# Kernel optimization log

Measured on AMD Instinct MI355X. Metric: run time of the kernel, lower is better.

Reference implementation:

```python
import jax, jax.numpy as jnp
import numpy as np

D_MODEL = 48
SSM_RATIO = 2
D_INNER = D_MODEL * SSM_RATIO   # 96
D_STATE = 16
DT_RANK = -(-D_MODEL // 16)     # ceil(48/16) = 3
K = 4                           # 4 scan directions
LAP_ITERS = 10
LAP_TAU = 0.1
B, DD, HH, WW = 2, 20, 20, 20   # L = 8000 (even)


def _lap_kernel(c):
    k = np.zeros((3, 3, 3), dtype=np.float32)
    k[1, 1, 1] = -6.0
    k[0, 1, 1] = k[2, 1, 1] = 1.0
    k[1, 0, 1] = k[1, 2, 1] = 1.0
    k[1, 1, 0] = k[1, 1, 2] = 1.0
    return jnp.asarray(np.tile(k[None, None], (c, 1, 1, 1, 1)))  # (C,1,3,3,3)


def _dwconv3d(x, w):
    # x: (B,C,D,H,W), w: (C,1,3,3,3) depthwise
    return jax.lax.conv_general_dilated(
        x, w, (1, 1, 1), 'SAME',
        dimension_numbers=('NCDHW', 'OIDHW', 'NCDHW'),
        feature_group_count=x.shape[1])


def _directions(feat):
    # feat: (B,C,D,H,W) -> (B,4,C,L): forward, flipped-L, channel-flipped, cross
    Bb, C, Dd, Hh, Ww = feat.shape
    L = Dd * Hh * Ww
    f = feat.reshape(Bb, C, L)
    bwd = f[:, :, ::-1]
    cb = feat[:, ::-1].reshape(Bb, C, L)
    half = (L + 1) // 2            # L is even here
    front = np.arange(half)
    back = np.arange(half, L)[::-1]
    cross_idx = np.stack([front, back], axis=1).reshape(-1)[:L]
    cross = f[:, :, cross_idx]
    return jnp.stack([f, bwd, cb, cross], axis=1)


def _selective_scan(u, delta, A, Bs, Cs, Ds):
    # u, delta: (b,k,d,l); A: (k,d,n); Bs, Cs: (b,k,n,l); Ds: (k,d)
    dl = jnp.moveaxis(delta, -1, 0)  # (l,b,k,d)
    ul = jnp.moveaxis(u, -1, 0)
    Bl = jnp.moveaxis(Bs, -1, 0)     # (l,b,k,n)
    Cl = jnp.moveaxis(Cs, -1, 0)
    h0 = jnp.zeros(u.shape[:3] + (A.shape[-1],), u.dtype)  # (b,k,d,n)

    def step(h, inp):
        d_t, u_t, b_t, c_t = inp
        dA = jnp.exp(d_t[..., None] * A[None])                    # (b,k,d,n)
        h = dA * h + (d_t * u_t)[..., None] * b_t[:, :, None, :]  # (b,k,d,n)
        y = jnp.einsum('bkdn,bkn->bkd', h, c_t)
        return h, y

    _, ys = jax.lax.scan(step, h0, (dl, ul, Bl, Cl))
    y = jnp.moveaxis(ys, 0, -1)  # (b,k,d,l)
    return y + Ds[None, :, :, None] * u


def setup_inputs() -> dict:
    key = jax.random.key(0)
    ks = jax.random.split(key, 10)

    def rn(k, shape, scale=0.02):
        return jax.random.normal(k, shape, dtype=jnp.float32) * scale

    x = jax.random.normal(ks[0], (B, DD, HH, WW, D_MODEL), dtype=jnp.float32)
    in_proj_w = rn(ks[1], (2 * D_INNER, D_MODEL))
    in_proj_cross_w = rn(ks[2], (D_INNER, D_MODEL))
    conv_w = rn(ks[3], (D_INNER, 1, 3, 3, 3), 0.1)
    conv_b = jnp.zeros((D_INNER,), jnp.float32)
    x_proj_weight = rn(ks[4], (K, DT_RANK + 2 * D_STATE, D_INNER))
    dt_std = DT_RANK ** -0.5
    dt_projs_weight = jax.random.uniform(ks[5], (K, D_INNER, DT_RANK), minval=-dt_std, maxval=dt_std, dtype=jnp.float32)
    dt = jnp.exp(jax.random.uniform(ks[6], (K, D_INNER)) * (np.log(0.1) - np.log(0.001)) + np.log(0.001))
    dt = jnp.clip(dt, 1e-4, None)
    dt_projs_bias = dt + jnp.log(-jnp.expm1(-dt))  # inverse softplus
    A_logs = jnp.log(jnp.tile(jnp.arange(1, D_STATE + 1, dtype=jnp.float32)[None], (K * D_INNER, 1)))
    Ds = jnp.ones((K * D_INNER,), jnp.float32)
    out_norm_w = jnp.ones((D_INNER,), jnp.float32)
    out_norm_b = jnp.zeros((D_INNER,), jnp.float32)
    out_proj_w = rn(ks[7], (D_MODEL, D_INNER))
    concat_w = rn(ks[8], (D_MODEL, 2 * D_MODEL))
    concat_b = jnp.zeros((D_MODEL,), jnp.float32)
    return dict(x=x, in_proj_w=in_proj_w, in_proj_cross_w=in_proj_cross_w,
                conv_w=conv_w, conv_b=conv_b, x_proj_weight=x_proj_weight,
                dt_projs_weight=dt_projs_weight, dt_projs_bias=dt_projs_bias,
                A_logs=A_logs, Ds=Ds, out_norm_w=out_norm_w, out_norm_b=out_norm_b,
                out_proj_w=out_proj_w, concat_w=concat_w, concat_b=concat_b)


def reference(x, in_proj_w, in_proj_cross_w, conv_w, conv_b, x_proj_weight,
              dt_projs_weight, dt_projs_bias, A_logs, Ds, out_norm_w,
              out_norm_b, out_proj_w, concat_w, concat_b):
    Bb, Dd, Hh, Ww, C = x.shape
    L = Dd * Hh * Ww
    xch = jnp.moveaxis(x, -1, 1)  # (B,C,D,H,W)

    # --- 3D Laplacian frequency decomposition: u_{k+1} = u_k + tau * lap(u_k)
    lap_k = _lap_kernel(C)
    u = xch
    for _ in range(LAP_ITERS):
        u = u + LAP_TAU * _dwconv3d(u, lap_k)
    low, high = u, xch - u
    cat = jnp.concatenate([low, high], axis=1)  # (B,2C,D,H,W)
    # 1x1x1 conv 2C -> C
    x_f = jnp.einsum('bcdhw,oc->bodhw', cat, concat_w) + concat_b[None, :, None, None, None]

    # --- CSS3D(x, x_f)
    xz = x @ in_proj_w.T                       # (B,D,H,W,2*d_inner)
    xi, z = jnp.split(xz, 2, axis=-1)
    xc = jnp.moveaxis(x_f, 1, -1) @ in_proj_cross_w.T  # (B,D,H,W,d_inner)
    xi = jnp.moveaxis(xi, -1, 1)               # (B,d_inner,D,H,W)
    xi = jax.nn.silu(_dwconv3d(xi, conv_w) + conv_b[None, :, None, None, None])
    xc = jnp.moveaxis(xc, -1, 1)

    xs = _directions(xi)    # (B,4,d_inner,L)
    xcs = _directions(xc)

    x_dbl = jnp.einsum('bkdl,kcd->bkcl', xcs, x_proj_weight)
    dts = x_dbl[:, :, :DT_RANK]
    Bs = x_dbl[:, :, DT_RANK:DT_RANK + D_STATE]
    Cs = x_dbl[:, :, DT_RANK + D_STATE:]
    dts = jnp.einsum('bkrl,kdr->bkdl', dts, dt_projs_weight)
    delta = jax.nn.softplus(dts + dt_projs_bias[None, :, :, None])
    A = -jnp.exp(A_logs.reshape(K, D_INNER, D_STATE))

    y = _selective_scan(xs, delta, A, Bs, Cs, Ds.reshape(K, D_INNER))
    y = y.mean(axis=1).reshape(Bb, D_INNER, Dd, Hh, Ww)
    y = jnp.moveaxis(y, 1, -1)                 # (B,D,H,W,d_inner)

    mu = y.mean(-1, keepdims=True)
    var = ((y - mu) ** 2).mean(-1, keepdims=True)
    y = (y - mu) / jnp.sqrt(var + 1e-5) * out_norm_w + out_norm_b

    y = y * jax.nn.sigmoid(z)
    return y @ out_proj_w.T                    # (B,D,H,W,d_model)
```

## Files before the change

kernel.cpp:

```cpp
#include <hip/hip_runtime.h>
#include <hip/hip_bf16.h>

typedef __hip_bfloat16 bf16;
typedef unsigned short u16;

#define L_  8000
#define CM  48
#define DI  96
#define DST 16
#define BB  2
#define NC  64
#define CS  125

#define W_IPW    0
#define W_IPCW   9216
#define W_CW     13824
#define W_CB     16416
#define W_XPW    16512
#define W_DTW    29952
#define W_DTB    31104
#define W_ALOG   31488
#define W_DSP    37632
#define W_NW     38016
#define W_NB     38112
#define W_OPW    38208
#define W_CCW    42816
#define W_CCB    47424
#define W_CVT_END 47472
#define W_WU     47472
#define W_WX     52080
#define W_BC     56688
#define W_ZT     56784
#define W_XIRAW  1592784
#define W_XT     3128784
#define W_UT     3896784
#define W_DTS    1592784
#define W_P      1784784
#define W_HLOC   2571216
#define W_HSTART 3357648
#define W_XIT    4664784
#define W_XCT    6200784
#define W_Y      4664784
#define W_F32_END 7736784
#define H_UP 0
#define H_BS 6144000
#define H_CS 7168000
#define H_END 8192000
#define NEED_BYTES ((size_t)W_F32_END*4 + (size_t)H_END*2)

__device__ __forceinline__ float b2f(bf16 v){ return __bfloat162float(v); }
__device__ __forceinline__ float bf2f(u16 v){ return __uint_as_float(((unsigned)v) << 16); }
__device__ __forceinline__ u16   f2b(float f){ bf16 h = __float2bfloat16(f); return *(u16*)&h; }
__device__ __forceinline__ float softplus(float tv){
    return fmaxf(tv, 0.f) + __logf(1.f + __expf(-fabsf(tv)));
}
template<int CTRL>
__device__ __forceinline__ float dppadd(float v){
    int x = __builtin_amdgcn_update_dpp(0, __float_as_int(v), CTRL, 0xF, 0xF, true);
    return v + __int_as_float(x);
}
__device__ __forceinline__ int lperm(int k, int gl){
    if (k == 1) return L_-1-gl;
    if (k == 3) return (gl & 1) ? (L_-1-(gl>>1)) : (gl>>1);
    return gl;
}

__global__ __launch_bounds__(256) void k_xt(const void* __restrict__ xin,
                                            const u16* __restrict__ probe,
                                            float* __restrict__ xt){
    __shared__ float tileS[CM][65];
    int tile = blockIdx.x;
    int b = tile / 125, lt = (tile - b*125)*64;
    bool isb = (probe[0] != 0);
    for (int i = threadIdx.x; i < 64*CM; i += 256){
        int l = i / CM, c = i - (i/CM)*CM;
        size_t gi = ((size_t)b*L_ + lt + l)*CM + c;
        float v = isb ? b2f(((const bf16*)xin)[gi]) : ((const float*)xin)[gi];
        tileS[c][l] = v;
    }
    __syncthreads();
    for (int i = threadIdx.x; i < CM*64; i += 256){
        int c = i >> 6, l = i & 63;
        xt[((size_t)(b*CM + c))*L_ + lt + l] = tileS[c][l];
    }
}

struct CvtArgs { const void* src[15]; int beg[16]; };

__global__ __launch_bounds__(256) void k_cvt(CvtArgs a, float* __restrict__ dst){
    int i = blockIdx.x*256 + threadIdx.x;
    if (i >= W_CVT_END) return;
    bool isb = (((const u16*)a.src[9])[0] != 0);
    int s = 1;
    #pragma unroll
    for (int t = 2; t < 15; ++t) if (i >= a.beg[t]) s = t;
    int j = i - a.beg[s];
    dst[i] = isb ? b2f(((const bf16*)a.src[s])[j]) : ((const float*)a.src[s])[j];
}

__global__ __launch_bounds__(256) void k_zero_out(const u16* __restrict__ probe, void* out){
    int i = blockIdx.x*256 + threadIdx.x;
    if (i >= BB*L_*CM) return;
    if (probe[0] != 0) ((u16*)out)[i] = 0;
    else               ((unsigned*)out)[i] = 0;
}

__global__ __launch_bounds__(256) void k_prew(const float* __restrict__ ipcw,
                                              const float* __restrict__ ccw,
                                              const float* __restrict__ ccb,
                                              float* __restrict__ Wu, float* __restrict__ Wx,
                                              float* __restrict__ bc){
    int i = blockIdx.x*256 + threadIdx.x;
    if (i >= DI*CM) return;
    int j = i / CM, m = i - j*CM;
    float s1 = 0.f, s2 = 0.f;
    for (int o = 0; o < CM; ++o){
        float w = ipcw[j*CM + o];
        s1 = fmaf(w, ccw[o*DI + m],      s1);
        s2 = fmaf(w, ccw[o*DI + CM + m], s2);
    }
    Wx[i] = s2; Wu[i] = s1 - s2;
    if (m == 0){
        float sb = 0.f;
        for (int o = 0; o < CM; ++o) sb = fmaf(ipcw[j*CM + o], ccb[o], sb);
        bc[j] = sb;
    }
}

#define LSTR  24
#define LSLAB (22*LSTR)
__global__ __launch_bounds__(1024) void k_lap(const float* __restrict__ xt,
                                              float* __restrict__ ut){
    __shared__ float buf[2][22*LSLAB];
    int bc = blockIdx.x;
    for (int i = threadIdx.x; i < 2*22*LSLAB; i += 1024) ((float*)buf)[i] = 0.f;
    __syncthreads();
    const float* xp = xt + (size_t)bc*L_;
    for (int v = threadIdx.x; v < L_; v += 1024){
        int d = v/400, r = v - 400*d, h = r/20, w = r - 20*h;
        buf[0][(d+1)*LSLAB + (h+1)*LSTR + (w+2)] = xp[v];
    }
    __syncthreads();
    int cur = 0;
    for (int it = 0; it < 10; ++it){
        int nxt = cur ^ 1;
        const float* bcur = buf[cur];
        float* bnxt = buf[nxt];
        for (int tk = threadIdx.x; tk < 2000; tk += 1024){
            int d = tk/100; int rem = tk - 100*d; int h = rem/5; int w0 = (rem - 5*h)*4;
            int base = (d+1)*LSLAB + (h+1)*LSTR + (w0+2);
            float2 c01 = *(const float2*)&bcur[base];
            float2 c23 = *(const float2*)&bcur[base+2];
            float  eL  = bcur[base-1], eR = bcur[base+4];
            float2 u01 = *(const float2*)&bcur[base-LSTR],  u23 = *(const float2*)&bcur[base-LSTR+2];
            float2 d01 = *(const float2*)&bcur[base+LSTR],  d23 = *(const float2*)&bcur[base+LSTR+2];
            float2 m01 = *(const float2*)&bcur[base-LSLAB], m23 = *(const float2*)&bcur[base-LSLAB+2];
            float2 p01 = *(const float2*)&bcur[base+LSLAB], p23 = *(const float2*)&bcur[base+LSLAB+2];
            float s0 = eL    + c01.y + u01.x + d01.x + m01.x + p01.x;
            float s1 = c01.x + c23.x + u01.y + d01.y + m01.y + p01.y;
            float s2 = c01.y + c23.y + u23.x + d23.x + m23.x + p23.x;
            float s3 = c23.x + eR    + u23.y + d23.y + m23.y + p23.y;
            float2 r01, r23;
            r01.x = fmaf(0.1f, s0 - 6.f*c01.x, c01.x);
            r01.y = fmaf(0.1f, s1 - 6.f*c01.y, c01.y);
            r23.x = fmaf(0.1f, s2 - 6.f*c23.x, c23.x);
            r23.y = fmaf(0.1f, s3 - 6.f*c23.y, c23.y);
            *(float2*)&bnxt[base]   = r01;
            *(float2*)&bnxt[base+2] = r23;
        }
        __syncthreads();
        cur = nxt;
    }
    float* uo = ut + (size_t)bc*L_;
    for (int v = threadIdx.x; v < L_; v += 1024){
        int d = v/400, r = v - 400*d, h = r/20, w = r - 20*h;
        uo[v] = buf[cur][(d+1)*LSLAB + (h+1)*LSTR + (w+2)];
    }
}

__global__ __launch_bounds__(256) void k_proj_xz(const float* __restrict__ xt,
                                                 const float* __restrict__ ipw,
                                                 float* __restrict__ xi_raw,
                                                 float* __restrict__ zt){
    __shared__ float w[DI*CM];
    int jh = blockIdx.y;
    for (int i = threadIdx.x; i < DI*CM; i += 256) w[i] = ipw[jh*DI*CM + i];
    __syncthreads();
    int sub = threadIdx.x >> 6;
    int lane = threadIdx.x & 63;
    int v = blockIdx.x*64 + lane;
    int b = v / L_, l = v - b*L_;
    float xv[CM];
    #pragma unroll
    for (int c = 0; c < CM; ++c) xv[c] = xt[((size_t)(b*CM + c))*L_ + l];
    float* dst = (jh == 0) ? xi_raw : zt;
    for (int jj = 0; jj < 24; ++jj){
        int j = sub*24 + jj;
        float s = 0.f;
        #pragma unroll
        for (int c = 0; c < CM; ++c) s = fmaf(w[j*CM + c], xv[c], s);
        dst[((size_t)(b*DI + j))*L_ + l] = s;
    }
}

__global__ __launch_bounds__(256) void k_proj_xc(const float* __restrict__ xt,
                                                 const float* __restrict__ ut,
                                                 const float* __restrict__ Wu,
                                                 const float* __restrict__ Wx,
                                                 const float* __restrict__ bc,
                                                 float* __restrict__ xct){
    __shared__ float wu_s[48*CM], wx_s[48*CM], bc_s[48];
    int jh = blockIdx.y;
    for (int i = threadIdx.x; i < 48*CM; i += 256){
        wu_s[i] = Wu[jh*48*CM + i];
        wx_s[i] = Wx[jh*48*CM + i];
    }
    if (threadIdx.x < 48) bc_s[threadIdx.x] = bc[jh*48 + threadIdx.x];
    __syncthreads();
    int sub = threadIdx.x >> 6;
    int lane = threadIdx.x & 63;
    int v = blockIdx.x*64 + lane;
    int b = v / L_, l = v - b*L_;
    float uv[CM], xv[CM];
    #pragma unroll
    for (int c = 0; c < CM; ++c){
        uv[c] = ut[((size_t)(b*CM + c))*L_ + l];
        xv[c] = xt[((size_t)(b*CM + c))*L_ + l];
    }
    for (int jj = 0; jj < 12; ++jj){
        int jl = sub*12 + jj;
        float s = bc_s[jl];
        #pragma unroll
        for (int m = 0; m < CM; ++m){
            s = fmaf(wu_s[jl*CM + m], uv[m], s);
            s = fmaf(wx_s[jl*CM + m], xv[m], s);
        }
        xct[((size_t)(b*DI + jh*48 + jl))*L_ + l] = s;
    }
}

__global__ __launch_bounds__(512) void k_conv(const float* __restrict__ xi_raw,
                                              const float* __restrict__ cwv,
                                              const float* __restrict__ cbv,
                                              float* __restrict__ xit){
    __shared__ float in_s[L_];
    int bc = blockIdx.x;
    int b = bc / DI, c = bc - b*DI;
    const float* src = xi_raw + (size_t)bc*L_;
    for (int v = threadIdx.x; v < L_; v += 512) in_s[v] = src[v];
    float w[27];
    #pragma unroll
    for (int i = 0; i < 27; ++i) w[i] = cwv[c*27 + i];
    float bias = cbv[c];
    __syncthreads();
    float* dst = xit + (size_t)bc*L_;
    for (int v = threadIdx.x; v < L_; v += 512){
        int d = v / 400; int r = v - d*400; int h = r / 20; int ww = r - h*20;
        float s = bias;
        #pragma unroll
        for (int kd = 0; kd < 3; ++kd){
            int dd = d + kd - 1; if (dd < 0 || dd > 19) continue;
            #pragma unroll
            for (int kh = 0; kh < 3; ++kh){
                int hh = h + kh - 1; if (hh < 0 || hh > 19) continue;
                #pragma unroll
                for (int kw = 0; kw < 3; ++kw){
                    int wv = ww + kw - 1; if (wv < 0 || wv > 19) continue;
                    s = fmaf(w[kd*9+kh*3+kw], in_s[(dd*20+hh)*20+wv], s);
                }
            }
        }
        float sig = 1.f / (1.f + __expf(-s));
        dst[v] = s * sig;
    }
}

__global__ __launch_bounds__(256) void k_xdbl(const float* __restrict__ xct,
                                              const float* __restrict__ xit,
                                              const float* __restrict__ xpw,
                                              float* __restrict__ dts,
                                              u16* __restrict__ up,
                                              u16* __restrict__ Bso,
                                              u16* __restrict__ Cso){
    __shared__ float xpw_s[36*DI];
    __shared__ float xct_s[DI*64];
    int bk = blockIdx.y, b = bk >> 2, k = bk & 3;
    int lt = blockIdx.x*64;
    int t = threadIdx.x;
    bool flip = (k == 2);
    for (int i = t; i < 36*DI; i += 256) xpw_s[i] = (i < 35*DI) ? xpw[(size_t)k*35*DI + i] : 0.f;
    for (int i = t; i < DI*64; i += 256){
        int dd = i >> 6, l = i & 63;
        int ls = lperm(k, lt + l);
        int dp = flip ? (DI-1-dd) : dd;
        xct_s[((dd >> 2)*64 + l)*4 + (dd & 3)] = xct[((size_t)(b*DI + dp))*L_ + ls];
    }
    __syncthreads();
    int sub = t >> 6, l = t & 63, gl = lt + l;
    float acc[9];
    #pragma unroll
    for (int j = 0; j < 9; ++j) acc[j] = 0.f;
    for (int dd4 = 0; dd4 < 24; ++dd4){
        float4 v = *(const float4*)&xct_s[(dd4*64 + l)*4];
        #pragma unroll
        for (int j = 0; j < 9; ++j){
            float4 w = *(const float4*)&xpw_s[(sub*9 + j)*DI + dd4*4];
            acc[j] = fmaf(v.x, w.x, fmaf(v.y, w.y, fmaf(v.z, w.z, fmaf(v.w, w.w, acc[j]))));
        }
    }
    #pragma unroll
    for (int j = 0; j < 9; ++j){
        int c = sub*9 + j;
        if (c < 3)       dts[((size_t)bk*3 + c)*L_ + gl] = acc[j];
        else if (c < 19) Bso[((size_t)bk*DST + (c-3))*L_ + gl]  = f2b(acc[j]);
        else if (c < 35) Cso[((size_t)bk*DST + (c-19))*L_ + gl] = f2b(acc[j]);
    }
    for (int i = t; i < DI*64; i += 256){
        int dd = i >> 6, l2 = i & 63;
        int ls = lperm(k, lt + l2);
        int dp = flip ? (DI-1-dd) : dd;
        up[((size_t)bk*DI + dd)*L_ + lt + l2] = f2b(xit[((size_t)(b*DI + dp))*L_ + ls]);
    }
}

#define SCAN_LDS 24096
template<int PASS>
__global__ __launch_bounds__(192) void k_scan(const float* __restrict__ dts,
                                              const float* __restrict__ dtw,
                                              const float* __restrict__ dtb,
                                              const float* __restrict__ alog,
                                              const float* __restrict__ dsp,
                                              const u16* __restrict__ up,
                                              const u16* __restrict__ bs_g,
                                              const u16* __restrict__ cs_g,
                                              const float* __restrict__ hstart,
                                              float* __restrict__ P,
                                              float* __restrict__ Hloc,
                                              u16* __restrict__ y_g){
    extern __shared__ char smem[];
    float* dts4 = (float*)smem;
    u16*   bc_s = (u16*)(smem + 2000);
    u16*   u_s  = (u16*)(smem + 12000);

    int chunk = blockIdx.x, bk = blockIdx.y, dg = blockIdx.z;
    int t = threadIdx.x, k = bk & 3;
    size_t dtsbase = (size_t)bk*3*L_ + (size_t)chunk*CS;
    for (int i = t; i < CS; i += 192){
        float4 v;
        v.x = dts[dtsbase + i];
        v.y = dts[dtsbase + L_ + i];
        v.z = dts[dtsbase + 2*L_ + i];
        v.w = 0.f;
        *(float4*)&dts4[i*4] = v;
    }
    size_t bcb = ((size_t)bk*DST)*L_ + (size_t)chunk*CS;
    for (int i = t; i < DST*CS; i += 192){
        int n = i/CS, col = i - n*CS;
        bc_s[col*40 + n] = bs_g[bcb + (size_t)n*L_ + col];
        if (PASS == 3) bc_s[col*40 + 16 + n] = cs_g[bcb + (size_t)n*L_ + col];
    }
    size_t upb = ((size_t)bk*DI + dg*48)*L_ + (size_t)chunk*CS;
    for (int i = t; i < 48*CS; i += 192){
        int dl = i/CS, col = i - dl*CS;
        u_s[dl*126 + col] = up[upb + (size_t)dl*L_ + col];
    }
    int dloc = t >> 2, nq = t & 3, d = dg*48 + dloc;
    int gd = k*DI + d;
    float w0 = dtw[gd*3], w1 = dtw[gd*3+1], w2 = dtw[gd*3+2], bia = dtb[gd];
    float a2[4];
    #pragma unroll
    for (int j = 0; j < 4; ++j)
        a2[j] = -__expf(alog[gd*DST + nq*4 + j]) * 1.44269504f;
    float dsD = dsp[gd];
    float h[4];
    if (PASS == 1){
        #pragma unroll
        for (int j = 0; j < 4; ++j) h[j] = 0.f;
    } else {
        float4 hv = *(const float4*)&hstart[(((size_t)(bk*NC + chunk))*DI + d)*DST + nq*4];
        h[0] = hv.x; h[1] = hv.y; h[2] = hv.z; h[3] = hv.w;
    }
    float S = 0.f;
    __syncthreads();

    const u16* ur = u_s + dloc*126;
    u16* yrow = y_g + ((size_t)bk*L_ + (size_t)chunk*CS)*DI + d;

    for (int l = 0; l < CS; ++l){
        float4 dt4 = *(const float4*)&dts4[l*4];
        float tv = fmaf(dt4.x, w0, fmaf(dt4.y, w1, fmaf(dt4.z, w2, bia)));
        float ds = softplus(tv);
        float uu = bf2f(ur[l]);
        float dsu = ds * uu;
        ushort4 bv = *(const ushort4*)&bc_s[l*40 + nq*4];
        float e[4];
        #pragma unroll
        for (int j = 0; j < 4; ++j) e[j] = __builtin_amdgcn_exp2f(ds * a2[j]);
        h[0] = fmaf(e[0], h[0], dsu * bf2f(bv.x));
        h[1] = fmaf(e[1], h[1], dsu * bf2f(bv.y));
        h[2] = fmaf(e[2], h[2], dsu * bf2f(bv.z));
        h[3] = fmaf(e[3], h[3], dsu * bf2f(bv.w));
        if (PASS == 1){
            S += ds;
        } else {
            ushort4 cv = *(const ushort4*)&bc_s[l*40 + 16 + nq*4];
            float y = h[0]*bf2f(cv.x);
            y = fmaf(h[1], bf2f(cv.y), y);
            y = fmaf(h[2], bf2f(cv.z), y);
            y = fmaf(h[3], bf2f(cv.w), y);
            y = dppadd<0xB1>(y);
            y = dppadd<0x4E>(y);
            if (nq == 0) yrow[(size_t)l*DI] = f2b(fmaf(dsD, uu, y));
        }
    }
    if (PASS == 1){
        size_t idx = (((size_t)(bk*NC + chunk))*DI + d)*DST + nq*4;
        float4 pv, hv;
        pv.x = __builtin_amdgcn_exp2f(S*a2[0]); pv.y = __builtin_amdgcn_exp2f(S*a2[1]);
        pv.z = __builtin_amdgcn_exp2f(S*a2[2]); pv.w = __builtin_amdgcn_exp2f(S*a2[3]);
        hv.x = h[0]; hv.y = h[1]; hv.z = h[2]; hv.w = h[3];
        *(float4*)&P[idx] = pv;
        *(float4*)&Hloc[idx] = hv;
    }
}

__global__ __launch_bounds__(256) void k_scan_mid(const float* __restrict__ P,
                                                  const float* __restrict__ Hloc,
                                                  float* __restrict__ Hstart){
    int blk = blockIdx.x;
    int bk = blk / 6, s = blk - bk*6;
    int t = threadIdx.x;
    size_t base = (size_t)bk*NC*DI*DST + s*256 + t;
    float h = 0.f;
    float pq[8], lq[8];
    #pragma unroll
    for (int j = 0; j < 8; ++j){ pq[j] = P[base + (size_t)j*1536]; lq[j] = Hloc[base + (size_t)j*1536]; }
    for (int c = 0; c < NC; ++c){
        float pn = 0.f, ln = 0.f;
        if (c + 8 < NC){
            pn = P[base + (size_t)(c+8)*1536];
            ln = Hloc[base + (size_t)(c+8)*1536];
        }
        size_t cb = base + (size_t)c*1536;
        Hstart[cb] = h;
        int r = c & 7;
        h = fmaf(pq[r], h, lq[r]);
        pq[r] = pn; lq[r] = ln;
    }
}

__global__ __launch_bounds__(256) void k_final(const u16* __restrict__ y,
                                               const float* __restrict__ zt,
                                               const float* __restrict__ nw,
                                               const float* __restrict__ nb,
                                               const float* __restrict__ opw,
                                               const u16* __restrict__ probe,
                                               void* __restrict__ out){
    __shared__ float opw_s[CM*100];
    __shared__ float ynorm[32*100];
    __shared__ float nw_s[DI], nb_s[DI];
    __shared__ u16   ostage[32*CM];
    for (int i = threadIdx.x; i < CM*DI; i += 256){
        int o = i / DI, dd = i - o*DI;
        opw_s[o*100 + dd] = opw[i];
    }
    if (threadIdx.x < DI){ nw_s[threadIdx.x] = nw[threadIdx.x]; nb_s[threadIdx.x] = nb[threadIdx.x]; }
    __syncthreads();
    int t = threadIdx.x, sub = t & 7, vi = t >> 3;
    int v = blockIdx.x*32 + vi;
    int b = v / L_, l = v - b*L_;
    int dd0 = sub*12;
    float yv[12];
    #pragma unroll
    for (int j = 0; j < 12; ++j) yv[j] = 0.f;
    #pragma unroll
    for (int k = 0; k < 4; ++k){
        const u16* yp = y + (((size_t)(b*4 + k))*L_ + l)*DI + dd0;
        ushort4 aa = *(const ushort4*)yp;
        ushort4 bb = *(const ushort4*)(yp + 4);
        ushort4 cc = *(const ushort4*)(yp + 8);
        yv[0] += bf2f(aa.x); yv[1] += bf2f(aa.y); yv[2]  += bf2f(aa.z); yv[3]  += bf2f(aa.w);
        yv[4] += bf2f(bb.x); yv[5] += bf2f(bb.y); yv[6]  += bf2f(bb.z); yv[7]  += bf2f(bb.w);
        yv[8] += bf2f(cc.x); yv[9] += bf2f(cc.y); yv[10] += bf2f(cc.z); yv[11] += bf2f(cc.w);
    }
    float mu = 0.f;
    #pragma unroll
    for (int j = 0; j < 12; ++j){ yv[j] *= 0.25f; mu += yv[j]; }
    mu += __shfl_xor(mu, 1); mu += __shfl_xor(mu, 2); mu += __shfl_xor(mu, 4);
    mu *= (1.f/DI);
    float var = 0.f;
    #pragma unroll
    for (int j = 0; j < 12; ++j){ float tv = yv[j] - mu; var = fmaf(tv, tv, var); }
    var += __shfl_xor(var, 1); var += __shfl_xor(var, 2); var += __shfl_xor(var, 4);
    var *= (1.f/DI);
    float rstd = rsqrtf(var + 1e-5f);
    #pragma unroll
    for (int j = 0; j < 12; ++j){
        int dd = dd0 + j;
        float g = fmaf((yv[j] - mu)*rstd, nw_s[dd], nb_s[dd]);
        float zz = zt[((size_t)(b*DI + dd))*L_ + l];
        ynorm[vi*100 + dd] = g / (1.f + __expf(-zz));
    }
    __syncthreads();
    bool isb = (probe[0] != 0);
    #pragma unroll
    for (int oi = 0; oi < 6; ++oi){
        int o = sub*6 + oi;
        float s = 0.f;
        #pragma unroll
        for (int c = 0; c < 24; ++c){
            float4 yy = *(const float4*)&ynorm[vi*100 + c*4];
            float4 ww = *(const float4*)&opw_s[o*100 + c*4];
            s = fmaf(yy.x, ww.x, s); s = fmaf(yy.y, ww.y, s);
            s = fmaf(yy.z, ww.z, s); s = fmaf(yy.w, ww.w, s);
        }
        if (isb) ostage[vi*CM + o] = f2b(s);
        else     ((float*)out)[(size_t)v*CM + o] = s;
    }
    __syncthreads();
    if (isb){
        u16* orow = (u16*)out + (size_t)blockIdx.x*32*CM;
        for (int i = threadIdx.x; i < 32*CM; i += 256) orow[i] = ostage[i];
    }
}

extern "C" void kernel_launch(void* const* d_in, const int* in_sizes, int n_in,
                              void* d_out, int out_size, void* d_ws, size_t ws_size,
                              hipStream_t stream) {
    const u16* probe = (const u16*)d_in[9];

    if (ws_size < NEED_BYTES){
        k_zero_out<<<(BB*L_*CM + 255)/256, 256, 0, stream>>>(probe, d_out);
        return;
    }

    float* F  = (float*)d_ws;
    u16*  Hb  = (u16*)((char*)d_ws + (size_t)W_F32_END*4);
    u16*  up  = Hb + H_UP;
    u16*  bs  = Hb + H_BS;
    u16*  cs  = Hb + H_CS;
    u16*  yb  = (u16*)(F + W_Y);

    CvtArgs a;
    static const int beg[16] = {-1, W_IPW, W_IPCW, W_CW, W_CB, W_XPW, W_DTW, W_DTB,
                                W_ALOG, W_DSP, W_NW, W_NB, W_OPW, W_CCW, W_CCB, W_CVT_END};
    for (int i = 0; i < 15; ++i) a.src[i] = d_in[i];
    for (int i = 0; i < 16; ++i) a.beg[i] = beg[i];

    k_xt     <<<250, 256, 0, stream>>>(d_in[0], probe, F + W_XT);
    k_cvt    <<<(W_CVT_END + 255)/256, 256, 0, stream>>>(a, F);
    k_prew   <<<(DI*CM + 255)/256, 256, 0, stream>>>(F + W_IPCW, F + W_CCW, F + W_CCB,
                                                     F + W_WU, F + W_WX, F + W_BC);
    k_lap    <<<BB*CM, 1024, 0, stream>>>(F + W_XT, F + W_UT);
    k_proj_xz<<<dim3(250,2), 256, 0, stream>>>(F + W_XT, F + W_IPW, F + W_XIRAW, F + W_ZT);
    k_proj_xc<<<dim3(250,2), 256, 0, stream>>>(F + W_XT, F + W_UT, F + W_WU, F + W_WX, F + W_BC, F + W_XCT);
    k_conv   <<<BB*DI, 512, 0, stream>>>(F + W_XIRAW, F + W_CW, F + W_CB, F + W_XIT);
    k_xdbl   <<<dim3(125, BB*4), 256, 0, stream>>>(F + W_XCT, F + W_XIT, F + W_XPW,
                                                   F + W_DTS, up, bs, cs);
    k_scan<1><<<dim3(NC, BB*4, 2), 192, SCAN_LDS, stream>>>(F + W_DTS, F + W_DTW, F + W_DTB,
                                                            F + W_ALOG, F + W_DSP, up, bs, cs,
                                                            F + W_HSTART, F + W_P, F + W_HLOC, yb);
    k_scan_mid<<<BB*4*6, 256, 0, stream>>>(F + W_P, F + W_HLOC, F + W_HSTART);
    k_scan<3><<<dim3(NC, BB*4, 2), 192, SCAN_LDS, stream>>>(F + W_DTS, F + W_DTW, F + W_DTB,
                                                            F + W_ALOG, F + W_DSP, up, bs, cs,
                                                            F + W_HSTART, F + W_P, F + W_HLOC, yb);
    k_final  <<<500, 256, 0, stream>>>(yb, F + W_ZT, F + W_NW, F + W_NB, F + W_OPW, probe, d_out);
}
```

Measured before the change: 348.3 us.

## Merge setup kernels, precompute softplus table in scan, move D-skip into final

```diff
diff --git a/kernel.cpp b/kernel.cpp
--- a/kernel.cpp
+++ b/kernel.cpp
@@ -40,15 +40,14 @@
 #define W_HSTART 3357648
 #define W_XIT    4664784
 #define W_XCT    6200784
-#define W_Y      4664784
 #define W_F32_END 7736784
 #define H_UP 0
 #define H_BS 6144000
 #define H_CS 7168000
-#define H_END 8192000
+#define H_Y  8192000
+#define H_END 14336000
 #define NEED_BYTES ((size_t)W_F32_END*4 + (size_t)H_END*2)
 
-__device__ __forceinline__ float b2f(bf16 v){ return __bfloat162float(v); }
 __device__ __forceinline__ float bf2f(u16 v){ return __uint_as_float(((unsigned)v) << 16); }
 __device__ __forceinline__ u16   f2b(float f){ bf16 h = __float2bfloat16(f); return *(u16*)&h; }
 __device__ __forceinline__ float softplus(float tv){
@@ -64,38 +63,71 @@
     if (k == 3) return (gl & 1) ? (L_-1-(gl>>1)) : (gl>>1);
     return gl;
 }
-
-__global__ __launch_bounds__(256) void k_xt(const void* __restrict__ xin,
-                                            const u16* __restrict__ probe,
-                                            float* __restrict__ xt){
+__device__ __forceinline__ unsigned packh2(float a, float b){
+    _Float16 ha = (_Float16)a, hb = (_Float16)b;
+    u16 x, y;
+    __builtin_memcpy(&x, &ha, 2);
+    __builtin_memcpy(&y, &hb, 2);
+    return (unsigned)x | ((unsigned)y << 16);
+}
+__device__ __forceinline__ float h2f(u16 v){
+    _Float16 h;
+    __builtin_memcpy(&h, &v, 2);
+    return (float)h;
+}
+
+struct CvtArgs { const void* src[15]; int beg[16]; };
+
+__global__ __launch_bounds__(256) void k_head(CvtArgs a, float* __restrict__ F){
     __shared__ float tileS[CM][65];
-    int tile = blockIdx.x;
-    int b = tile / 125, lt = (tile - b*125)*64;
-    bool isb = (probe[0] != 0);
-    for (int i = threadIdx.x; i < 64*CM; i += 256){
-        int l = i / CM, c = i - (i/CM)*CM;
-        size_t gi = ((size_t)b*L_ + lt + l)*CM + c;
-        float v = isb ? b2f(((const bf16*)xin)[gi]) : ((const float*)xin)[gi];
-        tileS[c][l] = v;
-    }
-    __syncthreads();
-    for (int i = threadIdx.x; i < CM*64; i += 256){
-        int c = i >> 6, l = i & 63;
-        xt[((size_t)(b*CM + c))*L_ + lt + l] = tileS[c][l];
-    }
-}
-
-struct CvtArgs { const void* src[15]; int beg[16]; };
-
-__global__ __launch_bounds__(256) void k_cvt(CvtArgs a, float* __restrict__ dst){
-    int i = blockIdx.x*256 + threadIdx.x;
-    if (i >= W_CVT_END) return;
     bool isb = (((const u16*)a.src[9])[0] != 0);
-    int s = 1;
-    #pragma unroll
-    for (int t = 2; t < 15; ++t) if (i >= a.beg[t]) s = t;
-    int j = i - a.beg[s];
-    dst[i] = isb ? b2f(((const bf16*)a.src[s])[j]) : ((const float*)a.src[s])[j];
+    int blk = blockIdx.x, t = threadIdx.x;
+    if (blk < 250){
+        int b = blk / 125, lt = (blk - b*125)*64;
+        const void* xin = a.src[0];
+        for (int i = t; i < 64*CM; i += 256){
+            int l = i / CM, c = i - (i/CM)*CM;
+            size_t gi = ((size_t)b*L_ + lt + l)*CM + c;
+            tileS[c][l] = isb ? bf2f(((const u16*)xin)[gi]) : ((const float*)xin)[gi];
+        }
+        __syncthreads();
+        for (int i = t; i < CM*64; i += 256){
+            int c = i >> 6, l = i & 63;
+            F[W_XT + ((size_t)(b*CM + c))*L_ + lt + l] = tileS[c][l];
+        }
+    } else if (blk < 436){
+        int i = (blk - 250)*256 + t;
+        if (i >= W_CVT_END) return;
+        int s = 1;
+        #pragma unroll
+        for (int q = 2; q < 15; ++q) if (i >= a.beg[q]) s = q;
+        int j = i - a.beg[s];
+        F[i] = isb ? bf2f(((const u16*)a.src[s])[j]) : ((const float*)a.src[s])[j];
+    } else {
+        int i = (blk - 436)*256 + t;
+        if (i >= DI*CM) return;
+        int j = i / CM, m = i - j*CM;
+        const u16* ipcb = (const u16*)a.src[2];  const float* ipcf = (const float*)a.src[2];
+        const u16* ccwb = (const u16*)a.src[13]; const float* ccwf = (const float*)a.src[13];
+        const u16* ccbb = (const u16*)a.src[14]; const float* ccbf = (const float*)a.src[14];
+        float s1 = 0.f, s2 = 0.f;
+        for (int o = 0; o < CM; ++o){
+            float w  = isb ? bf2f(ipcb[j*CM + o])      : ipcf[j*CM + o];
+            float c1 = isb ? bf2f(ccwb[o*DI + m])      : ccwf[o*DI + m];
+            float c2 = isb ? bf2f(ccwb[o*DI + CM + m]) : ccwf[o*DI + CM + m];
+            s1 = fmaf(w, c1, s1); s2 = fmaf(w, c2, s2);
+        }
+        F[W_WX + i] = s2; F[W_WU + i] = s1 - s2;
+        if (m == 0){
+            float sb = 0.f;
+            for (int o = 0; o < CM; ++o){
+                float w = isb ? bf2f(ipcb[j*CM + o]) : ipcf[j*CM + o];
+                float c = isb ? bf2f(ccbb[o]) : ccbf[o];
+                sb = fmaf(w, c, sb);
+            }
+            F[W_BC + j] = sb;
+        }
+    }
 }
 
 __global__ __launch_bounds__(256) void k_zero_out(const u16* __restrict__ probe, void* out){
@@ -103,28 +135,6 @@
     if (i >= BB*L_*CM) return;
     if (probe[0] != 0) ((u16*)out)[i] = 0;
     else               ((unsigned*)out)[i] = 0;
-}
-
-__global__ __launch_bounds__(256) void k_prew(const float* __restrict__ ipcw,
-                                              const float* __restrict__ ccw,
-                                              const float* __restrict__ ccb,
-                                              float* __restrict__ Wu, float* __restrict__ Wx,
-                                              float* __restrict__ bc){
-    int i = blockIdx.x*256 + threadIdx.x;
-    if (i >= DI*CM) return;
-    int j = i / CM, m = i - j*CM;
-    float s1 = 0.f, s2 = 0.f;
-    for (int o = 0; o < CM; ++o){
-        float w = ipcw[j*CM + o];
-        s1 = fmaf(w, ccw[o*DI + m],      s1);
-        s2 = fmaf(w, ccw[o*DI + CM + m], s2);
-    }
-    Wx[i] = s2; Wu[i] = s1 - s2;
-    if (m == 0){
-        float sb = 0.f;
-        for (int o = 0; o < CM; ++o) sb = fmaf(ipcw[j*CM + o], ccb[o], sb);
-        bc[j] = sb;
-    }
 }
 
 #define LSTR  24
@@ -178,64 +188,59 @@
     }
 }
 
-__global__ __launch_bounds__(256) void k_proj_xz(const float* __restrict__ xt,
-                                                 const float* __restrict__ ipw,
-                                                 float* __restrict__ xi_raw,
-                                                 float* __restrict__ zt){
-    __shared__ float w[DI*CM];
-    int jh = blockIdx.y;
-    for (int i = threadIdx.x; i < DI*CM; i += 256) w[i] = ipw[jh*DI*CM + i];
-    __syncthreads();
+__global__ __launch_bounds__(256) void k_proj(const float* __restrict__ xt,
+                                              const float* __restrict__ ut,
+                                              const float* __restrict__ ipw,
+                                              const float* __restrict__ Wu,
+                                              const float* __restrict__ Wx,
+                                              const float* __restrict__ bcv,
+                                              float* __restrict__ xi_raw,
+                                              float* __restrict__ zt,
+                                              float* __restrict__ xct){
+    __shared__ float sw[4672];
+    int role = blockIdx.y;
     int sub = threadIdx.x >> 6;
     int lane = threadIdx.x & 63;
     int v = blockIdx.x*64 + lane;
     int b = v / L_, l = v - b*L_;
-    float xv[CM];
-    #pragma unroll
-    for (int c = 0; c < CM; ++c) xv[c] = xt[((size_t)(b*CM + c))*L_ + l];
-    float* dst = (jh == 0) ? xi_raw : zt;
-    for (int jj = 0; jj < 24; ++jj){
-        int j = sub*24 + jj;
-        float s = 0.f;
-        #pragma unroll
-        for (int c = 0; c < CM; ++c) s = fmaf(w[j*CM + c], xv[c], s);
-        dst[((size_t)(b*DI + j))*L_ + l] = s;
-    }
-}
-
-__global__ __launch_bounds__(256) void k_proj_xc(const float* __restrict__ xt,
-                                                 const float* __restrict__ ut,
-                                                 const float* __restrict__ Wu,
-                                                 const float* __restrict__ Wx,
-                                                 const float* __restrict__ bc,
-                                                 float* __restrict__ xct){
-    __shared__ float wu_s[48*CM], wx_s[48*CM], bc_s[48];
-    int jh = blockIdx.y;
-    for (int i = threadIdx.x; i < 48*CM; i += 256){
-        wu_s[i] = Wu[jh*48*CM + i];
-        wx_s[i] = Wx[jh*48*CM + i];
-    }
-    if (threadIdx.x < 48) bc_s[threadIdx.x] = bc[jh*48 + threadIdx.x];
-    __syncthreads();
-    int sub = threadIdx.x >> 6;
-    int lane = threadIdx.x & 63;
-    int v = blockIdx.x*64 + lane;
-    int b = v / L_, l = v - b*L_;
-    float uv[CM], xv[CM];
-    #pragma unroll
-    for (int c = 0; c < CM; ++c){
-        uv[c] = ut[((size_t)(b*CM + c))*L_ + l];
-        xv[c] = xt[((size_t)(b*CM + c))*L_ + l];
-    }
-    for (int jj = 0; jj < 12; ++jj){
-        int jl = sub*12 + jj;
-        float s = bc_s[jl];
-        #pragma unroll
-        for (int m = 0; m < CM; ++m){
-            s = fmaf(wu_s[jl*CM + m], uv[m], s);
-            s = fmaf(wx_s[jl*CM + m], xv[m], s);
-        }
-        xct[((size_t)(b*DI + jh*48 + jl))*L_ + l] = s;
+    if (role < 2){
+        for (int i = threadIdx.x; i < DI*CM; i += 256) sw[i] = ipw[role*DI*CM + i];
+        __syncthreads();
+        float xv[CM];
+        #pragma unroll
+        for (int c = 0; c < CM; ++c) xv[c] = xt[((size_t)(b*CM + c))*L_ + l];
+        float* dst = (role == 0) ? xi_raw : zt;
+        for (int jj = 0; jj < 24; ++jj){
+            int j = sub*24 + jj;
+            float s = 0.f;
+            #pragma unroll
+            for (int c = 0; c < CM; ++c) s = fmaf(sw[j*CM + c], xv[c], s);
+            dst[((size_t)(b*DI + j))*L_ + l] = s;
+        }
+    } else {
+        int jh = role - 2;
+        for (int i = threadIdx.x; i < 48*CM; i += 256){
+            sw[i] = Wu[jh*48*CM + i];
+            sw[2304 + i] = Wx[jh*48*CM + i];
+        }
+        if (threadIdx.x < 48) sw[4608 + threadIdx.x] = bcv[jh*48 + threadIdx.x];
+        __syncthreads();
+        float uv[CM], xv[CM];
+        #pragma unroll
+        for (int c = 0; c < CM; ++c){
+            uv[c] = ut[((size_t)(b*CM + c))*L_ + l];
+            xv[c] = xt[((size_t)(b*CM + c))*L_ + l];
+        }
+        for (int jj = 0; jj < 12; ++jj){
+            int jl = sub*12 + jj;
+            float s = sw[4608 + jl];
+            #pragma unroll
+            for (int m = 0; m < CM; ++m){
+                s = fmaf(sw[jl*CM + m], uv[m], s);
+                s = fmaf(sw[2304 + jl*CM + m], xv[m], s);
+            }
+            xct[((size_t)(b*DI + jh*48 + jl))*L_ + l] = s;
+        }
     }
 }
 
@@ -323,13 +328,12 @@
     }
 }
 
-#define SCAN_LDS 24096
+#define SCAN_LDS 36960
 template<int PASS>
 __global__ __launch_bounds__(192) void k_scan(const float* __restrict__ dts,
                                               const float* __restrict__ dtw,
                                               const float* __restrict__ dtb,
                                               const float* __restrict__ alog,
-                                              const float* __restrict__ dsp,
                                               const u16* __restrict__ up,
                                               const u16* __restrict__ bs_g,
                                               const u16* __restrict__ cs_g,
@@ -338,9 +342,10 @@
                                               float* __restrict__ Hloc,
                                               u16* __restrict__ y_g){
     extern __shared__ char smem[];
-    float* dts4 = (float*)smem;
-    u16*   bc_s = (u16*)(smem + 2000);
-    u16*   u_s  = (u16*)(smem + 12000);
+    float*    dts4 = (float*)smem;
+    float*    dtwb = (float*)(smem + 2000);
+    u16*      bc_s = (u16*)(smem + 2768);
+    unsigned* tab  = (unsigned*)(smem + 12768);
 
     int chunk = blockIdx.x, bk = blockIdx.y, dg = blockIdx.z;
     int t = threadIdx.x, k = bk & 3;
@@ -353,25 +358,35 @@
         v.w = 0.f;
         *(float4*)&dts4[i*4] = v;
     }
+    if (t < 48){
+        int gd = k*DI + dg*48 + t;
+        float4 wv;
+        wv.x = dtw[gd*3]; wv.y = dtw[gd*3+1]; wv.z = dtw[gd*3+2]; wv.w = dtb[gd];
+        *(float4*)&dtwb[t*4] = wv;
+    }
     size_t bcb = ((size_t)bk*DST)*L_ + (size_t)chunk*CS;
     for (int i = t; i < DST*CS; i += 192){
         int n = i/CS, col = i - n*CS;
         bc_s[col*40 + n] = bs_g[bcb + (size_t)n*L_ + col];
         if (PASS == 3) bc_s[col*40 + 16 + n] = cs_g[bcb + (size_t)n*L_ + col];
     }
+    __syncthreads();
     size_t upb = ((size_t)bk*DI + dg*48)*L_ + (size_t)chunk*CS;
     for (int i = t; i < 48*CS; i += 192){
         int dl = i/CS, col = i - dl*CS;
-        u_s[dl*126 + col] = up[upb + (size_t)dl*L_ + col];
+        float4 wv = *(const float4*)&dtwb[dl*4];
+        float4 d4 = *(const float4*)&dts4[col*4];
+        float tv = fmaf(d4.x, wv.x, fmaf(d4.y, wv.y, fmaf(d4.z, wv.z, wv.w)));
+        float ds = softplus(tv);
+        float uu = bf2f(up[upb + (size_t)dl*L_ + col]);
+        tab[dl*126 + col] = packh2(ds, ds*uu);
     }
     int dloc = t >> 2, nq = t & 3, d = dg*48 + dloc;
     int gd = k*DI + d;
-    float w0 = dtw[gd*3], w1 = dtw[gd*3+1], w2 = dtw[gd*3+2], bia = dtb[gd];
     float a2[4];
     #pragma unroll
     for (int j = 0; j < 4; ++j)
         a2[j] = -__expf(alog[gd*DST + nq*4 + j]) * 1.44269504f;
-    float dsD = dsp[gd];
     float h[4];
     if (PASS == 1){
         #pragma unroll
@@ -383,15 +398,13 @@
     float S = 0.f;
     __syncthreads();
 
-    const u16* ur = u_s + dloc*126;
+    const unsigned* tr = tab + dloc*126;
     u16* yrow = y_g + ((size_t)bk*L_ + (size_t)chunk*CS)*DI + d;
 
     for (int l = 0; l < CS; ++l){
-        float4 dt4 = *(const float4*)&dts4[l*4];
-        float tv = fmaf(dt4.x, w0, fmaf(dt4.y, w1, fmaf(dt4.z, w2, bia)));
-        float ds = softplus(tv);
-        float uu = bf2f(ur[l]);
-        float dsu = ds * uu;
+        unsigned w = tr[l];
+        float ds  = h2f((u16)(w & 0xffff));
+        float dsu = h2f((u16)(w >> 16));
         ushort4 bv = *(const ushort4*)&bc_s[l*40 + nq*4];
         float e[4];
         #pragma unroll
@@ -410,7 +423,7 @@
             y = fmaf(h[3], bf2f(cv.w), y);
             y = dppadd<0xB1>(y);
             y = dppadd<0x4E>(y);
-            if (nq == 0) yrow[(size_t)l*DI] = f2b(fmaf(dsD, uu, y));
+            if (nq == 0) yrow[(size_t)l*DI] = f2b(y);
         }
     }
     if (PASS == 1){
@@ -450,7 +463,9 @@
 }
 
 __global__ __launch_bounds__(256) void k_final(const u16* __restrict__ y,
+                                               const float* __restrict__ xit,
                                                const float* __restrict__ zt,
+                                               const float* __restrict__ Dsp,
                                                const float* __restrict__ nw,
                                                const float* __restrict__ nb,
                                                const float* __restrict__ opw,
@@ -458,17 +473,22 @@
                                                void* __restrict__ out){
     __shared__ float opw_s[CM*100];
     __shared__ float ynorm[32*100];
+    __shared__ float dsc_s[4*DI];
     __shared__ float nw_s[DI], nb_s[DI];
     __shared__ u16   ostage[32*CM];
     for (int i = threadIdx.x; i < CM*DI; i += 256){
         int o = i / DI, dd = i - o*DI;
         opw_s[o*100 + dd] = opw[i];
     }
+    for (int i = threadIdx.x; i < 4*DI; i += 256) dsc_s[i] = Dsp[i];
     if (threadIdx.x < DI){ nw_s[threadIdx.x] = nw[threadIdx.x]; nb_s[threadIdx.x] = nb[threadIdx.x]; }
     __syncthreads();
     int t = threadIdx.x, sub = t & 7, vi = t >> 3;
     int v = blockIdx.x*32 + vi;
     int b = v / L_, l = v - b*L_;
+    int lsrc[4];
+    lsrc[0] = l; lsrc[1] = L_-1-l; lsrc[2] = l;
+    lsrc[3] = (l & 1) ? (L_-1-(l>>1)) : (l>>1);
     int dd0 = sub*12;
     float yv[12];
     #pragma unroll
@@ -482,6 +502,12 @@
         yv[0] += bf2f(aa.x); yv[1] += bf2f(aa.y); yv[2]  += bf2f(aa.z); yv[3]  += bf2f(aa.w);
         yv[4] += bf2f(bb.x); yv[5] += bf2f(bb.y); yv[6]  += bf2f(bb.z); yv[7]  += bf2f(bb.w);
         yv[8] += bf2f(cc.x); yv[9] += bf2f(cc.y); yv[10] += bf2f(cc.z); yv[11] += bf2f(cc.w);
+        #pragma unroll
+        for (int j = 0; j < 12; ++j){
+            int dd = dd0 + j;
+            int dx = (k == 2) ? (DI-1-dd) : dd;
+            yv[j] = fmaf(dsc_s[k*DI + dd], xit[((size_t)(b*DI + dx))*L_ + lsrc[k]], yv[j]);
+        }
     }
     float mu = 0.f;
     #pragma unroll
@@ -539,7 +565,7 @@
     u16*  up  = Hb + H_UP;
     u16*  bs  = Hb + H_BS;
     u16*  cs  = Hb + H_CS;
-    u16*  yb  = (u16*)(F + W_Y);
+    u16*  yb  = Hb + H_Y;
 
     CvtArgs a;
     static const int beg[16] = {-1, W_IPW, W_IPCW, W_CW, W_CB, W_XPW, W_DTW, W_DTB,
@@ -547,22 +573,21 @@
     for (int i = 0; i < 15; ++i) a.src[i] = d_in[i];
     for (int i = 0; i < 16; ++i) a.beg[i] = beg[i];
 
-    k_xt     <<<250, 256, 0, stream>>>(d_in[0], probe, F + W_XT);
-    k_cvt    <<<(W_CVT_END + 255)/256, 256, 0, stream>>>(a, F);
-    k_prew   <<<(DI*CM + 255)/256, 256, 0, stream>>>(F + W_IPCW, F + W_CCW, F + W_CCB,
-                                                     F + W_WU, F + W_WX, F + W_BC);
+    k_head   <<<454, 256, 0, stream>>>(a, F);
     k_lap    <<<BB*CM, 1024, 0, stream>>>(F + W_XT, F + W_UT);
-    k_proj_xz<<<dim3(250,2), 256, 0, stream>>>(F + W_XT, F + W_IPW, F + W_XIRAW, F + W_ZT);
-    k_proj_xc<<<dim3(250,2), 256, 0, stream>>>(F + W_XT, F + W_UT, F + W_WU, F + W_WX, F + W_BC, F + W_XCT);
+    k_proj   <<<dim3(250,4), 256, 0, stream>>>(F + W_XT, F + W_UT, F + W_IPW,
+                                               F + W_WU, F + W_WX, F + W_BC,
+                                               F + W_XIRAW, F + W_ZT, F + W_XCT);
     k_conv   <<<BB*DI, 512, 0, stream>>>(F + W_XIRAW, F + W_CW, F + W_CB, F + W_XIT);
     k_xdbl   <<<dim3(125, BB*4), 256, 0, stream>>>(F + W_XCT, F + W_XIT, F + W_XPW,
                                                    F + W_DTS, up, bs, cs);
     k_scan<1><<<dim3(NC, BB*4, 2), 192, SCAN_LDS, stream>>>(F + W_DTS, F + W_DTW, F + W_DTB,
-                                                            F + W_ALOG, F + W_DSP, up, bs, cs,
+                                                            F + W_ALOG, up, bs, cs,
                                                             F + W_HSTART, F + W_P, F + W_HLOC, yb);
     k_scan_mid<<<BB*4*6, 256, 0, stream>>>(F + W_P, F + W_HLOC, F + W_HSTART);
     k_scan<3><<<dim3(NC, BB*4, 2), 192, SCAN_LDS, stream>>>(F + W_DTS, F + W_DTW, F + W_DTB,
-                                                            F + W_ALOG, F + W_DSP, up, bs, cs,
+                                                            F + W_ALOG, up, bs, cs,
                                                             F + W_HSTART, F + W_P, F + W_HLOC, yb);
-    k_final  <<<500, 256, 0, stream>>>(yb, F + W_ZT, F + W_NW, F + W_NB, F + W_OPW, probe, d_out);
-}
+    k_final  <<<500, 256, 0, stream>>>(yb, F + W_XIT, F + W_ZT, F + W_DSP, F + W_NW, F + W_NB,
+                                       F + W_OPW, probe, d_out);
+}
```

Result: faster. 340.8 us (-2.2%).
